# Kernel tuning notes

Measured on AMD Instinct MI355X. Metric: run time of the kernel, lower is better.

The kernel has to match this reference:

```python
import jax, jax.numpy as jnp
import numpy as np
from jax import lax

DIM = 180; NH = 6; WH = 16; WW = 16; MH = 8; MW = 8
HD = DIM // (2 * NH)  # 15, head dim; also the (non-sqrt) scale
RMS_EPS = 1.1920929e-07  # torch.finfo(float32).eps (RMSNorm eps=None)

def _conv(x, w, b, pad):
    # x: NHWC, w: HWIO
    return lax.conv_general_dilated(x, w, (1, 1), [(pad, pad), (pad, pad)],
                                    dimension_numbers=('NHWC', 'HWIO', 'NHWC')) + b

def _lrelu(x):
    return jnp.where(x >= 0, x, 0.2 * x)

def _ln(x, w, b, eps=1e-5):
    m = x.mean(-1, keepdims=True)
    v = jnp.mean((x - m) ** 2, -1, keepdims=True)
    return (x - m) / jnp.sqrt(v + eps) * w + b

def _forward(x, dfe_w1, dfe_b1, dfe_w2, dfe_b2, dfe_w3, dfe_b3, dfe_lw, dfe_lb,
             sl_w, sl_b, pos_pw, pos_pb, ln1w, ln1b, l1w, l1b, ln2w, ln2b,
             l2w, l2b, ln3w, ln3b, l3w, l3b, proj_w, proj_b, norm_w):
    B, C, H, W = x.shape
    xh = jnp.transpose(x, (0, 2, 3, 1))  # NHWC
    shortcut = xh
    # DFE: conv branch gated by 1x1 linear branch
    h = _lrelu(_conv(xh, dfe_w1, dfe_b1, 0))
    h = _lrelu(_conv(h, dfe_w2, dfe_b2, 1))
    h = _conv(h, dfe_w3, dfe_b3, 0)
    qv = h * _conv(xh, dfe_lw, dfe_lb, 0)  # (B,H,W,C)
    # window partition
    L = WH * WW
    qv = qv.reshape(B, H // WH, WH, W // WW, WW, C).transpose(0, 1, 3, 2, 4, 5).reshape(-1, L, C)
    Bw = qv.shape[0]
    qv = qv.reshape(Bw, L, 2, NH, HD).transpose(2, 0, 3, 1, 4)
    q, v = qv[0], qv[1]  # (Bw, NH, L, HD)
    # spatial linear projection of v: downsample window -> base window
    rH, rW = WH // MH, WW // MW
    vp = v.reshape(Bw, NH, MH, rH, MW, rW, HD).transpose(0, 1, 2, 4, 6, 3, 5)
    vp = vp.reshape(Bw, NH, MH * MW, HD, rH * rW)
    vp = ((vp @ sl_w) + sl_b)[..., 0]  # (Bw, NH, mapL, HD)
    corr = jnp.einsum('bhlc,bhmc->bhlm', q, vp) / HD  # (Bw, NH, L, mapL)
    # dynamic relative position bias
    bh = jnp.arange(1 - WH, WH, dtype=jnp.float32)
    bw = jnp.arange(1 - WW, WW, dtype=jnp.float32)
    biases = jnp.stack(jnp.meshgrid(bh, bw, indexing='ij')).reshape(2, -1).T  # (nb, 2)
    p = biases @ pos_pw + pos_pb
    p = jax.nn.relu(_ln(p, ln1w, ln1b)) @ l1w + l1b
    p = jax.nn.relu(_ln(p, ln2w, ln2b)) @ l2w + l2b
    pos = jax.nn.relu(_ln(p, ln3w, ln3b)) @ l3w + l3b  # (nb, NH)
    coords = jnp.stack(jnp.meshgrid(jnp.arange(WH), jnp.arange(WW), indexing='ij')).reshape(2, -1)
    rel = coords[:, :, None] - coords[:, None, :]  # (2, L, L)
    idx = (rel[0] + WH - 1) * (2 * WW - 1) + (rel[1] + WW - 1)  # (L, L)
    rpb = pos[idx.reshape(-1)].reshape(L, MH, rH, MW, rW, NH)
    rpb = rpb.transpose(0, 1, 3, 5, 2, 4).reshape(L, MH * MW, NH, rH * rW).mean(-1)
    rpb = rpb.transpose(2, 0, 1)  # (NH, L, mapL)
    corr = corr + rpb[None]
    xs = jnp.einsum('bhlm,bhmc->bhlc', corr, vp).transpose(0, 2, 1, 3).reshape(Bw, L, NH * HD)
    # channel self-correlation
    qc = q.transpose(0, 2, 1, 3).reshape(Bw, L, NH * HD)
    vc = v.transpose(0, 2, 1, 3).reshape(Bw, L, NH * HD)
    cmap = jnp.einsum('blc,bld->bcd', qc, vc) / L  # (Bw, C/2, C/2)
    xc = jnp.einsum('bcd,bld->blc', cmap, vc)  # (Bw, L, C/2)
    # window reverse
    def wrev(win):
        c = win.shape[-1]
        return win.reshape(B, H // WH, W // WW, WH, WW, c).transpose(0, 1, 3, 2, 4, 5).reshape(B, H, W, c)
    xs = wrev(xs.reshape(Bw, WH, WW, NH * HD))
    xc = wrev(xc.reshape(Bw, WH, WW, NH * HD))
    y = jnp.concatenate([xs, xc], -1)  # (B, H, W, C)
    y = y @ proj_w + proj_b
    y = y * (1.0 / jnp.sqrt(jnp.mean(y * y, -1, keepdims=True) + RMS_EPS)) * norm_w
    y = shortcut + y
    return jnp.transpose(y, (0, 3, 1, 2))


def setup_inputs() -> dict:
    key = jax.random.key(0)
    ks = iter(jax.random.split(key, 32))
    def rn(shape, s=0.05):
        return jax.random.normal(next(ks), shape, jnp.float32) * s
    inp = {}
    inp['x'] = jax.random.normal(next(ks), (4, 180, 256, 256), jnp.float32)
    inp['dfe_w1'] = rn((1, 1, 180, 36)); inp['dfe_b1'] = rn((36,))
    inp['dfe_w2'] = rn((3, 3, 36, 36)); inp['dfe_b2'] = rn((36,))
    inp['dfe_w3'] = rn((1, 1, 36, 180)); inp['dfe_b3'] = rn((180,))
    inp['dfe_lw'] = rn((1, 1, 180, 180)); inp['dfe_lb'] = rn((180,))
    inp['sl_w'] = rn((4, 1)); inp['sl_b'] = rn((1,))
    inp['pos_pw'] = rn((2, 11)); inp['pos_pb'] = rn((11,))
    inp['ln1w'] = jnp.ones((11,)); inp['ln1b'] = jnp.zeros((11,))
    inp['l1w'] = rn((11, 11)); inp['l1b'] = rn((11,))
    inp['ln2w'] = jnp.ones((11,)); inp['ln2b'] = jnp.zeros((11,))
    inp['l2w'] = rn((11, 11)); inp['l2b'] = rn((11,))
    inp['ln3w'] = jnp.ones((11,)); inp['ln3b'] = jnp.zeros((11,))
    inp['l3w'] = rn((11, 6)); inp['l3b'] = rn((6,))
    inp['proj_w'] = rn((180, 180)); inp['proj_b'] = rn((180,))
    inp['norm_w'] = jnp.ones((180,))
    return inp


def reference(x, dfe_w1, dfe_b1, dfe_w2, dfe_b2, dfe_w3, dfe_b3, dfe_lw, dfe_lb,
              sl_w, sl_b, pos_pw, pos_pb, ln1w, ln1b, l1w, l1b, ln2w, ln2b,
              l2w, l2b, ln3w, ln3b, l3w, l3b, proj_w, proj_b, norm_w):
    return _forward(x, dfe_w1, dfe_b1, dfe_w2, dfe_b2, dfe_w3, dfe_b3, dfe_lw, dfe_lb,
                    sl_w, sl_b, pos_pw, pos_pb, ln1w, ln1b, l1w, l1b, ln2w, ln2b,
                    l2w, l2b, ln3w, ln3b, l3w, l3b, proj_w, proj_b, norm_w)
```

## Files before the change

kernel.cpp:

```cpp
#include <hip/hip_runtime.h>
#include <stdint.h>

typedef unsigned short u16;
typedef unsigned int   u32;

#define HW 65536

typedef __bf16 bf16x8 __attribute__((ext_vector_type(8)));
typedef float  f32x4  __attribute__((ext_vector_type(4)));

static __device__ __forceinline__ float bf2f(u16 h) {
    u32 u = ((u32)h) << 16;
    return __builtin_bit_cast(float, u);
}
static __device__ __forceinline__ u16 f2bf(float f) {
    u32 u = __builtin_bit_cast(u32, f);
    u += 0x7fffu + ((u >> 16) & 1u);
    return (u16)(u >> 16);
}
static __device__ __forceinline__ void bf2x2(u32 u, float& a, float& b) {
    a = __builtin_bit_cast(float, u << 16);
    b = __builtin_bit_cast(float, u & 0xffff0000u);
}
static __device__ __forceinline__ f32x4 mfma16(bf16x8 a, bf16x8 b, f32x4 c) {
    return __builtin_amdgcn_mfma_f32_16x16x32_bf16(a, b, c, 0, 0, 0);
}

static __device__ __forceinline__ void lnrelu11(float* p, const float* __restrict__ w,
                                                const float* __restrict__ b) {
    float m = 0.f;
    #pragma unroll
    for (int k = 0; k < 11; k++) m += p[k];
    m *= (1.0f / 11.0f);
    float v = 0.f;
    #pragma unroll
    for (int k = 0; k < 11; k++) { float d = p[k] - m; v = fmaf(d, d, v); }
    v *= (1.0f / 11.0f);
    float r = 1.0f / sqrtf(v + 1e-5f);
    #pragma unroll
    for (int k = 0; k < 11; k++) {
        float t = (p[k] - m) * r * w[k] + b[k];
        p[k] = t > 0.f ? t : 0.f;
    }
}

__global__ __launch_bounds__(1024) void k_pos(
    const float* __restrict__ pw, const float* __restrict__ pb,
    const float* __restrict__ ln1w, const float* __restrict__ ln1b,
    const float* __restrict__ l1w, const float* __restrict__ l1b,
    const float* __restrict__ ln2w, const float* __restrict__ ln2b,
    const float* __restrict__ l2w, const float* __restrict__ l2b,
    const float* __restrict__ ln3w, const float* __restrict__ ln3b,
    const float* __restrict__ l3w, const float* __restrict__ l3b,
    float* __restrict__ pos)
{
    int i = threadIdx.x;
    if (i >= 961) return;
    float b0 = (float)(i / 31) - 15.0f;
    float b1 = (float)(i % 31) - 15.0f;
    float p[11], t[11];
    #pragma unroll
    for (int j = 0; j < 11; j++) p[j] = b0 * pw[j] + b1 * pw[11 + j] + pb[j];
    lnrelu11(p, ln1w, ln1b);
    #pragma unroll
    for (int j = 0; j < 11; j++) {
        float s = l1b[j];
        #pragma unroll
        for (int k = 0; k < 11; k++) s = fmaf(p[k], l1w[k * 11 + j], s);
        t[j] = s;
    }
    lnrelu11(t, ln2w, ln2b);
    #pragma unroll
    for (int j = 0; j < 11; j++) {
        float s = l2b[j];
        #pragma unroll
        for (int k = 0; k < 11; k++) s = fmaf(t[k], l2w[k * 11 + j], s);
        p[j] = s;
    }
    lnrelu11(p, ln3w, ln3b);
    #pragma unroll
    for (int h = 0; h < 6; h++) {
        float s = l3b[h];
        #pragma unroll
        for (int k = 0; k < 11; k++) s = fmaf(p[k], l3w[k * 6 + h], s);
        pos[i * 6 + h] = s;
    }
}

__global__ __launch_bounds__(256) void k_rpb(const float* __restrict__ pos,
                                             float* __restrict__ rpb)
{
    int g = blockIdx.x * 256 + threadIdx.x;
    if (g >= 6 * 256 * 64) return;
    int h = g >> 14;
    int l = (g >> 6) & 255;
    int m = g & 63;
    int yl = l >> 4, xl = l & 15;
    int my = m >> 3, mx = m & 7;
    float s = 0.f;
    #pragma unroll
    for (int ry = 0; ry < 2; ry++) {
        #pragma unroll
        for (int rx = 0; rx < 2; rx++) {
            int y2 = my * 2 + ry, x2 = mx * 2 + rx;
            int idx = (yl - y2 + 15) * 31 + (xl - x2 + 15);
            s += pos[idx * 6 + h];
        }
    }
    rpb[g] = 0.25f * s;
}

__global__ __launch_bounds__(256) void k_conv1(const float* __restrict__ x,
                                               const float* __restrict__ w,
                                               const float* __restrict__ b,
                                               u16* __restrict__ h1)
{
    int pix = blockIdx.x * 256 + threadIdx.x;
    int bb = pix >> 16, sp = pix & 65535;
    float acc[36];
    #pragma unroll
    for (int j = 0; j < 36; j++) acc[j] = b[j];
    const float* xp = x + (size_t)bb * 180 * HW + sp;
    for (int c = 0; c < 180; c++) {
        float xv = xp[(size_t)c * HW];
        #pragma unroll
        for (int j = 0; j < 36; j++) acc[j] = fmaf(xv, w[c * 36 + j], acc[j]);
    }
    u16* hp = h1 + (size_t)bb * 36 * HW + sp;
    #pragma unroll
    for (int j = 0; j < 36; j++) {
        float v = acc[j];
        v = v >= 0.f ? v : 0.2f * v;
        hp[(size_t)j * HW] = f2bf(v);
    }
}

__global__ __launch_bounds__(256) void k_conv3(const u16* __restrict__ h1,
                                               const float* __restrict__ w,
                                               const float* __restrict__ b,
                                               u16* __restrict__ h2)
{
    int tx = threadIdx.x, ty = threadIdx.y;
    int x0 = blockIdx.x * 16 + tx;
    int y0 = blockIdx.y * 16 + ty;
    int bb = blockIdx.z;
    float acc[36];
    #pragma unroll
    for (int j = 0; j < 36; j++) acc[j] = b[j];
    const u16* base = h1 + (size_t)bb * 36 * HW;
    for (int ky = 0; ky < 3; ky++) {
        int yy = y0 + ky - 1;
        if (yy < 0 || yy >= 256) continue;
        for (int kx = 0; kx < 3; kx++) {
            int xx = x0 + kx - 1;
            if (xx < 0 || xx >= 256) continue;
            const u16* ip = base + yy * 256 + xx;
            const float* wp = w + ((ky * 3 + kx) * 36) * 36;
            for (int c = 0; c < 36; c++) {
                float v = bf2f(ip[(size_t)c * HW]);
                #pragma unroll
                for (int j = 0; j < 36; j++) acc[j] = fmaf(v, wp[c * 36 + j], acc[j]);
            }
        }
    }
    u16* op = h2 + (size_t)bb * 36 * HW + y0 * 256 + x0;
    #pragma unroll
    for (int j = 0; j < 36; j++) {
        float v = acc[j];
        v = v >= 0.f ? v : 0.2f * v;
        op[(size_t)j * HW] = f2bf(v);
    }
}

__global__ __launch_bounds__(256) void k_wgprep(const float* __restrict__ lw,
                                                const float* __restrict__ w3,
                                                u16* __restrict__ gwh,
                                                u16* __restrict__ gwl,
                                                u16* __restrict__ cwh,
                                                u16* __restrict__ cwl)
{
    int gidx = blockIdx.x * 256 + threadIdx.x;
    if (gidx < 36864) {
        int oc = gidx / 192, k = gidx % 192;
        float v = (oc < 180 && k < 180) ? lw[k * 180 + oc] : 0.f;
        u16 h = f2bf(v);
        float lo = v - bf2f(h);
        gwh[gidx] = h;
        gwl[gidx] = f2bf(lo);
    } else {
        int r = gidx - 36864;
        int oc = r / 64, k = r % 64;
        float v = (oc < 180 && k < 36) ? w3[k * 180 + oc] : 0.f;
        u16 h = f2bf(v);
        float lo = v - bf2f(h);
        cwh[r] = h;
        cwl[r] = f2bf(lo);
    }
}

__global__ __launch_bounds__(256) void k_gate(const u16* __restrict__ h2,
                                              const float* __restrict__ x,
                                              const u16* __restrict__ gwh,
                                              const u16* __restrict__ gwl,
                                              const u16* __restrict__ cwh,
                                              const u16* __restrict__ cwl,
                                              const float* __restrict__ b3,
                                              const float* __restrict__ lb,
                                              u16* __restrict__ qvT)
{
    __shared__ __align__(16) float xs[180 * 64];
    __shared__ __align__(16) u16  hs[36 * 64];
    int t = threadIdx.x;
    int lane = t & 63;
    int g = __builtin_amdgcn_readfirstlane(t >> 6);
    int m = lane & 15, q = lane >> 4;
    int blk = blockIdx.x;
    int w  = blk >> 2;
    int lq = blk & 3;
    int bb = w >> 8, wy = (w >> 4) & 15, wx = w & 15;
    int ocb = g * 48;
    int y0 = wy * 16 + lq * 4;
    int xc0 = wx * 16;
    const float* xb = x + (size_t)bb * 180 * HW;
    const u16*  hb = h2 + (size_t)bb * 36 * HW;

    for (int s = g; s < 45; s += 4) {
        int c = s * 4 + (lane >> 4);
        int swz = (c >> 3) & 1;
        int pp = (lane & 15) ^ (swz << 2);
        int p0 = pp * 4;
        int prow = p0 >> 4, pcol = p0 & 15;
        const float* gp = xb + (size_t)c * HW + (y0 + prow) * 256 + xc0 + pcol;
        __builtin_amdgcn_global_load_lds(
            (const __attribute__((address_space(1))) void*)gp,
            (__attribute__((address_space(3))) void*)(xs + s * 256),
            16, 0, 0);
    }
    for (int idx = t; idx < 288; idx += 256) {
        int c = idx >> 3, j = idx & 7;
        int p0 = j * 8;
        int prow = p0 >> 4, pcol = p0 & 15;
        uint4 v = *(const uint4*)(hb + (size_t)c * HW + (y0 + prow) * 256 + xc0 + pcol);
        int swz = (c >> 3) & 1;
        *(uint4*)(hs + c * 64 + (p0 ^ (swz << 4))) = v;
    }
    __syncthreads();

    f32x4 accG[3][4], accC[3][4];
    #pragma unroll
    for (int mt = 0; mt < 3; mt++)
        #pragma unroll
        for (int pt = 0; pt < 4; pt++) {
            f32x4 z = {0.f, 0.f, 0.f, 0.f};
            accG[mt][pt] = z;
            accC[mt][pt] = z;
        }

    #pragma unroll 2
    for (int ks = 0; ks < 6; ks++) {
        bf16x8 Bh[4], Bl[4];
        #pragma unroll
        for (int pt = 0; pt < 4; pt++)
            #pragma unroll
            for (int j = 0; j < 8; j++) {
                int c = ks * 32 + q * 8 + j;
                if (c > 179) c = 179;
                int p = pt * 16 + m;
                float v = xs[c * 64 + (p ^ (((c >> 3) & 1) << 4))];
                __bf16 hi = (__bf16)v;
                Bh[pt][j] = hi;
                Bl[pt][j] = (__bf16)(v - (float)hi);
            }
        #pragma unroll
        for (int mt = 0; mt < 3; mt++) {
            bf16x8 Ah = *(const bf16x8*)(gwh + (size_t)(ocb + mt * 16 + m) * 192 + ks * 32 + q * 8);
            bf16x8 Al = *(const bf16x8*)(gwl + (size_t)(ocb + mt * 16 + m) * 192 + ks * 32 + q * 8);
            #pragma unroll
            for (int pt = 0; pt < 4; pt++) {
                accG[mt][pt] = mfma16(Ah, Bh[pt], accG[mt][pt]);
                accG[mt][pt] = mfma16(Al, Bh[pt], accG[mt][pt]);
                accG[mt][pt] = mfma16(Ah, Bl[pt], accG[mt][pt]);
            }
        }
    }

    #pragma unroll
    for (int ks = 0; ks < 2; ks++) {
        bf16x8 B[4];
        #pragma unroll
        for (int pt = 0; pt < 4; pt++)
            #pragma unroll
            for (int j = 0; j < 8; j++) {
                int c = ks * 32 + q * 8 + j;
                if (c > 35) c = 35;
                int p = pt * 16 + m;
                B[pt][j] = __builtin_bit_cast(__bf16, hs[c * 64 + (p ^ (((c >> 3) & 1) << 4))]);
            }
        #pragma unroll
        for (int mt = 0; mt < 3; mt++) {
            bf16x8 Ah = *(const bf16x8*)(cwh + (size_t)(ocb + mt * 16 + m) * 64 + ks * 32 + q * 8);
            bf16x8 Al = *(const bf16x8*)(cwl + (size_t)(ocb + mt * 16 + m) * 64 + ks * 32 + q * 8);
            #pragma unroll
            for (int pt = 0; pt < 4; pt++) {
                accC[mt][pt] = mfma16(Ah, B[pt], accC[mt][pt]);
                accC[mt][pt] = mfma16(Al, B[pt], accC[mt][pt]);
            }
        }
    }

    __syncthreads();
    u16* qtile = (u16*)xs;
    #pragma unroll
    for (int mt = 0; mt < 3; mt++)
        #pragma unroll
        for (int r = 0; r < 4; r++) {
            int oc = ocb + mt * 16 + q * 4 + r;
            if (oc < 180) {
                float bc = b3[oc], bg = lb[oc];
                #pragma unroll
                for (int pt = 0; pt < 4; pt++) {
                    float ah = accC[mt][pt][r] + bc;
                    float al = accG[mt][pt][r] + bg;
                    qtile[oc * 66 + pt * 16 + m] = f2bf(ah * al);
                }
            }
        }
    __syncthreads();
    u16* qbase = qvT + (size_t)w * 180 * 256 + lq * 64;
    for (int i = t; i < 1440; i += 256) {
        int oc = i >> 3, ch = i & 7;
        *(uint4*)(qbase + (size_t)oc * 256 + ch * 8) =
            *(const uint4*)(qtile + oc * 66 + ch * 8);
    }
}

__global__ __launch_bounds__(256) void k_spat(const u16* __restrict__ qvT,
                                              const float* __restrict__ rpb,
                                              const float* __restrict__ slw,
                                              const float* __restrict__ slb,
                                              u16* __restrict__ yp)
{
    __shared__ __align__(16) float vp[6144];
    int w = blockIdx.x;
    int bb = w >> 8, wy = (w >> 4) & 15, wx = w & 15;
    int t = threadIdx.x;
    int lane = t & 63, wv = t >> 6;
    const u16* qw = qvT + (size_t)w * 180 * 256;
    float s0 = slw[0], s1 = slw[1], s2 = slw[2], s3 = slw[3], sb = slb[0];
    for (int o = t; o < 384; o += 256) vp[(o >> 6) * 1024 + (o & 63) * 16 + 15] = 0.f;
    for (int it = 0; it < 23; it++) {
        int p = wv + it * 4;
        if (p < 90) {
            int mm = lane;
            int l0 = (mm >> 3) * 32 + (mm & 7) * 2;
            const u16* rp2 = qw + (size_t)(90 + p) * 256;
            float s = sb + s0 * bf2f(rp2[l0]) + s1 * bf2f(rp2[l0 + 1])
                         + s2 * bf2f(rp2[l0 + 16]) + s3 * bf2f(rp2[l0 + 17]);
            vp[(p / 15) * 1024 + mm * 16 + (p % 15)] = s;
        }
    }
    __syncthreads();
    int l = t;
    size_t pixl = (size_t)((bb * 256 + wy * 16 + (l >> 4)) * 256 + wx * 16 + (l & 15));
    u16* op = yp + pixl * 192;
    ((u32*)op)[45] = 0u; ((u32*)op)[46] = 0u; ((u32*)op)[47] = 0u;
    for (int h = 0; h < 6; h++) {
        float q[16];
        #pragma unroll
        for (int d = 0; d < 15; d++) q[d] = bf2f(qw[(size_t)(h * 15 + d) * 256 + l]);
        q[15] = 0.f;
        float acc[16];
        #pragma unroll
        for (int d = 0; d < 16; d++) acc[d] = 0.f;
        const float* rp = rpb + ((h * 256 + l) << 6);
        const float4* vph = (const float4*)(vp + (h << 10));
        for (int m0 = 0; m0 < 64; m0 += 4) {
            float ra[4];
            *(float4*)ra = *(const float4*)(rp + m0);
            #pragma unroll
            for (int mm = 0; mm < 4; mm++) {
                int m = m0 + mm;
                float wvv[16];
                ((float4*)wvv)[0] = vph[m * 4 + 0];
                ((float4*)wvv)[1] = vph[m * 4 + 1];
                ((float4*)wvv)[2] = vph[m * 4 + 2];
                ((float4*)wvv)[3] = vph[m * 4 + 3];
                float s = 0.f;
                #pragma unroll
                for (int d2 = 0; d2 < 16; d2++) s = fmaf(q[d2], wvv[d2], s);
                s = s * (1.0f / 15.0f) + ra[mm];
                #pragma unroll
                for (int d2 = 0; d2 < 16; d2++) acc[d2] = fmaf(s, wvv[d2], acc[d2]);
            }
        }
        #pragma unroll
        for (int d = 0; d < 15; d++) op[h * 15 + d] = f2bf(acc[d]);
    }
}

__global__ __launch_bounds__(256) void k_chan(const u16* __restrict__ qvT,
                                              u16* __restrict__ yp)
{
    __shared__ __align__(16) u16 cm[96 * 104];
    __shared__ __align__(16) u16 xcb[128 * 104];
    int w = blockIdx.x;
    int bb = w >> 8, wy = (w >> 4) & 15, wx = w & 15;
    int t = threadIdx.x;
    int lane = t & 63, wv = t >> 6;
    int m = lane & 15, quad = lane >> 4;
    const u16* qw = qvT + (size_t)w * 180 * 256;

    int ct0 = (wv & 1) * 3, dt0 = (wv >> 1) * 3;
    f32x4 acc[3][3];
    #pragma unroll
    for (int i = 0; i < 3; i++)
        #pragma unroll
        for (int j = 0; j < 3; j++) {
            f32x4 z = {0.f, 0.f, 0.f, 0.f};
            acc[i][j] = z;
        }
    #pragma unroll
    for (int ks = 0; ks < 8; ks++) {
        bf16x8 A[3], B[3];
        #pragma unroll
        for (int i = 0; i < 3; i++)
            A[i] = *(const bf16x8*)(qw + (size_t)((ct0 + i) * 16 + m) * 256 + ks * 32 + quad * 8);
        #pragma unroll
        for (int j = 0; j < 3; j++) {
            int d = (dt0 + j) * 16 + m;
            int dd = d > 89 ? 89 : d;
            B[j] = *(const bf16x8*)(qw + (size_t)(90 + dd) * 256 + ks * 32 + quad * 8);
        }
        #pragma unroll
        for (int i = 0; i < 3; i++)
            #pragma unroll
            for (int j = 0; j < 3; j++)
                acc[i][j] = mfma16(A[i], B[j], acc[i][j]);
    }
    #pragma unroll
    for (int i = 0; i < 3; i++)
        #pragma unroll
        for (int j = 0; j < 3; j++)
            #pragma unroll
            for (int r = 0; r < 4; r++)
                cm[((ct0 + i) * 16 + quad * 4 + r) * 104 + (dt0 + j) * 16 + m] =
                    f2bf(acc[i][j][r] * (1.0f / 256.0f));
    __syncthreads();
    if (t < 96) {
        u32* z = (u32*)(cm + t * 104 + 90);
        z[0] = 0; z[1] = 0; z[2] = 0;
    }
    __syncthreads();

    int base_pix = (bb * 256 + wy * 16) * 256 + wx * 16;
    const __bf16* qwb = (const __bf16*)qw;
    for (int half = 0; half < 2; half++) {
        #pragma unroll
        for (int i = 0; i < 2; i++) {
            int ltl = wv * 2 + i;
            int lt = half * 8 + ltl;
            bf16x8 A[3];
            #pragma unroll
            for (int ks = 0; ks < 3; ks++) {
                const __bf16* colp = qwb + lt * 16 + m;
                #pragma unroll
                for (int j2 = 0; j2 < 8; j2++) {
                    int d = ks * 32 + quad * 8 + j2;
                    int dd = d > 89 ? 89 : d;
                    A[ks][j2] = colp[(size_t)(90 + dd) * 256];
                }
            }
            for (int ct = 0; ct < 6; ct++) {
                f32x4 c4 = {0.f, 0.f, 0.f, 0.f};
                #pragma unroll
                for (int ks = 0; ks < 3; ks++) {
                    bf16x8 B = *(const bf16x8*)(cm + (ct * 16 + m) * 104 + ks * 32 + quad * 8);
                    c4 = mfma16(A[ks], B, c4);
                }
                #pragma unroll
                for (int r = 0; r < 4; r++)
                    xcb[(ltl * 16 + quad * 4 + r) * 104 + ct * 16 + m] = f2bf(c4[r]);
            }
        }
        __syncthreads();
        #pragma unroll
        for (int it = 0; it < 6; it++) {
            int gg = t + it * 256;
            int lrow = gg / 12, seg = gg % 12;
            int l = half * 128 + lrow;
            int pix = base_pix + (l >> 4) * 256 + (l & 15);
            *(uint4*)(yp + (size_t)pix * 192 + 96 + seg * 8) =
                *(const uint4*)(xcb + lrow * 104 + seg * 8);
        }
        __syncthreads();
    }
}

__global__ __launch_bounds__(256) void k_wprep(const float* __restrict__ pjw,
                                               u16* __restrict__ whiT,
                                               u16* __restrict__ wloT)
{
    int g = blockIdx.x * 256 + threadIdx.x;
    int oc = g / 192, k = g % 192;
    int kp = -1;
    if (k < 90) kp = k;
    else if (k >= 96 && k <= 185) kp = k - 6;
    float v = (kp >= 0 && oc < 180) ? pjw[kp * 180 + oc] : 0.f;
    u16 h = f2bf(v);
    float lo = v - bf2f(h);
    whiT[g] = h;
    wloT[g] = f2bf(lo);
}

__global__ __launch_bounds__(256) void k_proj(const u16* __restrict__ yp,
                                              const float* __restrict__ x,
                                              const u16* __restrict__ whiT,
                                              const u16* __restrict__ wloT,
                                              const float* __restrict__ pb,
                                              const float* __restrict__ nw,
                                              float* __restrict__ out)
{
    __shared__ __align__(16) char smem[26112];
    __shared__ float part[4][4][16];
    u16*   ypl = (u16*)smem;
    float* st  = (float*)smem;
    int t = threadIdx.x;
    int lane = t & 63;
    int g = __builtin_amdgcn_readfirstlane(t >> 6);
    int m = lane & 15, q = lane >> 4;
    int pix0 = blockIdx.x * 64;
    int ocbase = g * 48;

    const char* ypc = (const char*)(yp + (size_t)pix0 * 192);
    int soff = (lane ^ ((lane >> 3) & 7)) << 4;
    for (int i = g; i < 24; i += 4) {
        __builtin_amdgcn_global_load_lds(
            (const __attribute__((address_space(1))) void*)(ypc + i * 1024 + soff),
            (__attribute__((address_space(3))) void*)(smem + i * 1024),
            16, 0, 0);
    }
    __syncthreads();

    f32x4 acc[3][4];
    #pragma unroll
    for (int mt = 0; mt < 3; mt++)
        #pragma unroll
        for (int pt = 0; pt < 4; pt++) {
            f32x4 z = {0.f, 0.f, 0.f, 0.f};
            acc[mt][pt] = z;
        }

    int mq = m * 24 + q;
    #pragma unroll 2
    for (int ks = 0; ks < 6; ks++) {
        bf16x8 B[4];
        #pragma unroll
        for (int pt = 0; pt < 4; pt++) {
            int G = pt * 384 + mq + ks * 4;
            int o = G & 63;
            int slot = (G & ~63) + (o ^ ((o >> 3) & 7));
            B[pt] = *(const bf16x8*)(ypl + slot * 8);
        }
        #pragma unroll
        for (int mt = 0; mt < 3; mt++) {
            bf16x8 Ah = *(const bf16x8*)(whiT + (size_t)(ocbase + mt * 16 + m) * 192 + ks * 32 + q * 8);
            bf16x8 Al = *(const bf16x8*)(wloT + (size_t)(ocbase + mt * 16 + m) * 192 + ks * 32 + q * 8);
            #pragma unroll
            for (int pt = 0; pt < 4; pt++) {
                acc[mt][pt] = mfma16(Ah, B[pt], acc[mt][pt]);
                acc[mt][pt] = mfma16(Al, B[pt], acc[mt][pt]);
            }
        }
    }

    float pbv[3][4], nwv[3][4];
    #pragma unroll
    for (int mt = 0; mt < 3; mt++)
        #pragma unroll
        for (int r = 0; r < 4; r++) {
            int oc = ocbase + mt * 16 + q * 4 + r;
            bool ok = oc < 180;
            pbv[mt][r] = ok ? pb[oc] : 0.f;
            nwv[mt][r] = ok ? nw[oc] : 0.f;
        }
    float ss[4] = {0.f, 0.f, 0.f, 0.f};
    #pragma unroll
    for (int mt = 0; mt < 3; mt++)
        #pragma unroll
        for (int pt = 0; pt < 4; pt++)
            #pragma unroll
            for (int r = 0; r < 4; r++) {
                float y = acc[mt][pt][r] + pbv[mt][r];
                acc[mt][pt][r] = y;
                ss[pt] = fmaf(y, y, ss[pt]);
            }
    #pragma unroll
    for (int pt = 0; pt < 4; pt++) {
        ss[pt] += __shfl_xor(ss[pt], 16);
        ss[pt] += __shfl_xor(ss[pt], 32);
    }
    if (q == 0) {
        #pragma unroll
        for (int pt = 0; pt < 4; pt++) part[g][pt][m] = ss[pt];
    }
    __syncthreads();
    float scale[4];
    #pragma unroll
    for (int pt = 0; pt < 4; pt++) {
        float tot = part[0][pt][m] + part[1][pt][m] + part[2][pt][m] + part[3][pt][m];
        scale[pt] = 1.0f / sqrtf(tot * (1.0f / 180.0f) + 1.1920929e-7f);
    }
    #pragma unroll
    for (int mt = 0; mt < 3; mt++)
        #pragma unroll
        for (int pt = 0; pt < 4; pt++)
            #pragma unroll
            for (int r = 0; r < 4; r++)
                acc[mt][pt][r] = acc[mt][pt][r] * scale[pt] * nwv[mt][r];

    int bb = pix0 >> 16, sp0 = pix0 & 65535;
    const float* xb = x + (size_t)bb * 180 * HW + sp0;
    float* ob = out + (size_t)bb * 180 * HW + sp0;
    #pragma unroll
    for (int ph = 0; ph < 2; ph++) {
        if ((g >> 1) == ph) {
            int rb = (g & 1) * 48;
            #pragma unroll
            for (int mt = 0; mt < 3; mt++)
                #pragma unroll
                for (int r = 0; r < 4; r++) {
                    int row = rb + mt * 16 + q * 4 + r;
                    #pragma unroll
                    for (int pt = 0; pt < 4; pt++)
                        st[row * 68 + pt * 16 + m] = acc[mt][pt][r];
                }
        }
        __syncthreads();
        int nch = ph ? 1344 : 1536;
        for (int i = t; i < nch; i += 256) {
            int row = i >> 4, j = i & 15;
            int oc = ph * 96 + row;
            f32x4 d = *(const f32x4*)(st + row * 68 + j * 4);
            size_t off = (size_t)oc * HW + j * 4;
            f32x4 xv = *(const f32x4*)(xb + off);
            *(f32x4*)(ob + off) = d + xv;
        }
        __syncthreads();
    }
}

extern "C" void kernel_launch(void* const* d_in, const int* in_sizes, int n_in,
                              void* d_out, int out_size, void* d_ws, size_t ws_size,
                              hipStream_t stream)
{
    const float* x    = (const float*)d_in[0];
    const float* w1   = (const float*)d_in[1];
    const float* b1   = (const float*)d_in[2];
    const float* w2   = (const float*)d_in[3];
    const float* b2   = (const float*)d_in[4];
    const float* w3   = (const float*)d_in[5];
    const float* b3   = (const float*)d_in[6];
    const float* lw   = (const float*)d_in[7];
    const float* lb   = (const float*)d_in[8];
    const float* slw  = (const float*)d_in[9];
    const float* slb  = (const float*)d_in[10];
    const float* pw   = (const float*)d_in[11];
    const float* pb   = (const float*)d_in[12];
    const float* ln1w = (const float*)d_in[13];
    const float* ln1b = (const float*)d_in[14];
    const float* l1w  = (const float*)d_in[15];
    const float* l1b  = (const float*)d_in[16];
    const float* ln2w = (const float*)d_in[17];
    const float* ln2b = (const float*)d_in[18];
    const float* l2w  = (const float*)d_in[19];
    const float* l2b  = (const float*)d_in[20];
    const float* ln3w = (const float*)d_in[21];
    const float* ln3b = (const float*)d_in[22];
    const float* l3w  = (const float*)d_in[23];
    const float* l3b  = (const float*)d_in[24];
    const float* pjw  = (const float*)d_in[25];
    const float* pjb  = (const float*)d_in[26];
    const float* nw   = (const float*)d_in[27];
    float* out = (float*)d_out;

    char* ws = (char*)d_ws;
    float* pos = (float*)(ws + 0);
    float* rpb = (float*)(ws + 24576);
    u16*  h2  = (u16*)(ws + 417792);
    u16*  whiT = (u16*)(ws + 417792);
    u16*  wloT = (u16*)(ws + 417792 + 73728);
    u16*  h1  = (u16*)(ws + 19292160);
    u16*  qvT = (u16*)(ws + 19292160);
    u16*  yp  = (u16*)(ws + 113664000);
    u16*  gwh = (u16*)(ws + 113664000);
    u16*  gwl = (u16*)(ws + 113664000 + 73728);
    u16*  cwh = (u16*)(ws + 113664000 + 147456);
    u16*  cwl = (u16*)(ws + 113664000 + 172032);

    k_wgprep<<<dim3(192), dim3(256), 0, stream>>>(lw, w3, gwh, gwl, cwh, cwl);
    k_pos<<<dim3(1), dim3(1024), 0, stream>>>(pw, pb, ln1w, ln1b, l1w, l1b,
                                              ln2w, ln2b, l2w, l2b, ln3w, ln3b,
                                              l3w, l3b, pos);
    k_rpb<<<dim3(384), dim3(256), 0, stream>>>(pos, rpb);
    k_conv1<<<dim3(1024), dim3(256), 0, stream>>>(x, w1, b1, h1);
    k_conv3<<<dim3(16, 16, 4), dim3(16, 16), 0, stream>>>(h1, w2, b2, h2);
    k_gate<<<dim3(4096), dim3(256), 0, stream>>>(h2, x, gwh, gwl, cwh, cwl,
                                                 b3, lb, qvT);
    k_wprep<<<dim3(144), dim3(256), 0, stream>>>(pjw, whiT, wloT);
    k_spat<<<dim3(1024), dim3(256), 0, stream>>>(qvT, rpb, slw, slb, yp);
    k_chan<<<dim3(1024), dim3(256), 0, stream>>>(qvT, yp);
    k_proj<<<dim3(4096), dim3(256), 0, stream>>>(yp, x, whiT, wloT, pjb, nw, out);
}
```

Baseline: 1.025 ms.

## Double-buffer x channel chunks in LDS for k_gate GEMM

Replaces the single up-front staging of all 180 input channels into LDS with 32-channel chunks in two ping-pong buffers. The async global-to-LDS load of the next chunk is issued while the current chunk is converted and fed to MFMA, with a barrier after each iteration. This cuts the kernel's LDS footprint from about 50KB to 24KB, which may allow more resident blocks, and overlaps memory latency with compute. The cost is six extra block barriers and dropping the unroll-by-2 on the k loop.

Result: no change. 1.038 ms (+1.3%).

```diff
diff --git a/kernel.cpp b/kernel.cpp
--- a/kernel.cpp
+++ b/kernel.cpp
@@ -198,6 +198,26 @@
     }
 }
 
+static __device__ __forceinline__ void stage_chunk(
+    const float* __restrict__ xb, int y0, int xc0, int ck,
+    float* __restrict__ dst, int g, int lane)
+{
+    int smax = (ck == 5) ? 5 : 8;
+    for (int s = g; s < smax; s += 4) {
+        int cl = s * 4 + (lane >> 4);
+        int cg = ck * 32 + cl;
+        int swz = (cl >> 3) & 1;
+        int pp = (lane & 15) ^ (swz << 2);
+        int p0 = pp * 4;
+        int prow = p0 >> 4, pcol = p0 & 15;
+        const float* gp = xb + (size_t)cg * HW + (y0 + prow) * 256 + xc0 + pcol;
+        __builtin_amdgcn_global_load_lds(
+            (const __attribute__((address_space(1))) void*)gp,
+            (__attribute__((address_space(3))) void*)(dst + s * 256),
+            16, 0, 0);
+    }
+}
+
 __global__ __launch_bounds__(256) void k_gate(const u16* __restrict__ h2,
                                               const float* __restrict__ x,
                                               const u16* __restrict__ gwh,
@@ -208,8 +228,11 @@
                                               const float* __restrict__ lb,
                                               u16* __restrict__ qvT)
 {
-    __shared__ __align__(16) float xs[180 * 64];
-    __shared__ __align__(16) u16  hs[36 * 64];
+    __shared__ __align__(16) char smem[24576];
+    float* buf0 = (float*)smem;
+    float* buf1 = (float*)(smem + 8192);
+    u16*  hs   = (u16*)(smem + 16384);
+
     int t = threadIdx.x;
     int lane = t & 63;
     int g = __builtin_amdgcn_readfirstlane(t >> 6);
@@ -224,18 +247,7 @@
     const float* xb = x + (size_t)bb * 180 * HW;
     const u16*  hb = h2 + (size_t)bb * 36 * HW;
 
-    for (int s = g; s < 45; s += 4) {
-        int c = s * 4 + (lane >> 4);
-        int swz = (c >> 3) & 1;
-        int pp = (lane & 15) ^ (swz << 2);
-        int p0 = pp * 4;
-        int prow = p0 >> 4, pcol = p0 & 15;
-        const float* gp = xb + (size_t)c * HW + (y0 + prow) * 256 + xc0 + pcol;
-        __builtin_amdgcn_global_load_lds(
-            (const __attribute__((address_space(1))) void*)gp,
-            (__attribute__((address_space(3))) void*)(xs + s * 256),
-            16, 0, 0);
-    }
+    stage_chunk(xb, y0, xc0, 0, buf0, g, lane);
     for (int idx = t; idx < 288; idx += 256) {
         int c = idx >> 3, j = idx & 7;
         int p0 = j * 8;
@@ -256,17 +268,19 @@
             accC[mt][pt] = z;
         }
 
-    #pragma unroll 2
     for (int ks = 0; ks < 6; ks++) {
+        if (ks < 5)
+            stage_chunk(xb, y0, xc0, ks + 1, (ks & 1) ? buf0 : buf1, g, lane);
+        const float* bufc = (ks & 1) ? buf1 : buf0;
         bf16x8 Bh[4], Bl[4];
         #pragma unroll
         for (int pt = 0; pt < 4; pt++)
             #pragma unroll
             for (int j = 0; j < 8; j++) {
-                int c = ks * 32 + q * 8 + j;
-                if (c > 179) c = 179;
+                int cl = q * 8 + j;
+                if (ks == 5 && cl > 19) cl = 19;
                 int p = pt * 16 + m;
-                float v = xs[c * 64 + (p ^ (((c >> 3) & 1) << 4))];
+                float v = bufc[cl * 64 + (p ^ (((cl >> 3) & 1) << 4))];
                 __bf16 hi = (__bf16)v;
                 Bh[pt][j] = hi;
                 Bl[pt][j] = (__bf16)(v - (float)hi);
@@ -282,6 +296,7 @@
                 accG[mt][pt] = mfma16(Ah, Bl[pt], accG[mt][pt]);
             }
         }
+        __syncthreads();
     }
 
     #pragma unroll
@@ -309,7 +324,7 @@
     }
 
     __syncthreads();
-    u16* qtile = (u16*)xs;
+    u16* qtile = (u16*)smem;
     #pragma unroll
     for (int mt = 0; mt < 3; mt++)
         #pragma unroll
```
